# Kernel optimization log

Measured on AMD Instinct MI355X. Metric: run time of the kernel, lower is better.

The kernel has to match this reference:

```python
import jax, jax.numpy as jnp
import numpy as np

KERNEL_SIZE = 7  # must be odd
PAD = KERNEL_SIZE // 2


def setup_inputs() -> dict:
    key = jax.random.key(0)
    k1, k2 = jax.random.split(key)
    B, C, H, W = 8, 128, 256, 256
    x = jax.random.normal(k1, (B, C, H, W), dtype=jnp.float32)
    y = jax.random.normal(k2, (B, C, H, W), dtype=jnp.float32)
    return {"x": x, "y": y}


def reference(x, y):
    # x, y: [B, C, H, W] -> coef: [B, K*K, H, W]
    B, C, H, W = x.shape
    ypad = jnp.pad(y, ((0, 0), (0, 0), (PAD, PAD), (PAD, PAD)))  # ZeroPad2d
    coefs = []
    for i in range(KERNEL_SIZE):
        for j in range(KERNEL_SIZE):
            # shifted window of y, same spatial size as x
            yw = ypad[:, :, i:i + H, j:j + W]
            coefs.append(jnp.sum(x * yw, axis=1))  # channel dot product -> [B, H, W]
    return jnp.stack(coefs, axis=1)  # [B, K*K, H, W]
```

## Files before the change

kernel.cpp:

```cpp
#include <hip/hip_runtime.h>


#define Bq 8
#define Cq 128
#define Hq 256
#define Wq 256
#define Kq 7
#define TILE_H 8
#define TILE_W 64
#define NTHR 448

__global__ __launch_bounds__(NTHR)
void corr7_kernel(const float* __restrict__ x, const float* __restrict__ y,
                  float* __restrict__ out)
{
    const int t    = threadIdx.x;
    const int wave = t >> 6;
    const int lane = t & 63;
    const int lw   = lane & 7;
    const int lr   = lane >> 3;

    int bid = (int)blockIdx.x;
    bid = (bid & 7) * 128 + (bid >> 3);

    const int tw = bid & 3;
    const int th = (bid >> 2) & 31;
    const int b  = bid >> 7;

    const int h0 = th * TILE_H;
    const int w0 = tw * TILE_W;

    const size_t cs   = (size_t)Hq * Wq;
    const size_t base = (size_t)b * Cq * cs;

    const float* xp = x + base + (size_t)(h0 + lr) * Wq + (w0 + 8 * lw);

    const int gy    = h0 + lr + wave - 3;
    const bool rowok = (unsigned)gy < (unsigned)Hq;
    const float rowm = rowok ? 1.f : 0.f;
    const int gyc   = gy < 0 ? 0 : (gy > Hq - 1 ? Hq - 1 : gy);
    const float* yrow0 = y + base + (size_t)gyc * Wq;

    const int lanem1 = (lane + 63) & 63;
    const int lanep1 = (lane + 1) & 63;
    const bool isL = (lw == 0);
    const bool isR = (lw == 7);
    const float lm = (rowok && tw > 0) ? 1.f : 0.f;
    const float rm = (rowok && tw < 3) ? 1.f : 0.f;
    const int loff = (tw > 0) ? (w0 - 4) : w0;
    const int roff = (tw < 3) ? (w0 + TILE_W) : w0;

    float acc[Kq][8];
#pragma unroll
    for (int j = 0; j < Kq; ++j)
#pragma unroll
        for (int r = 0; r < 8; ++r) acc[j][r] = 0.f;

    for (int c = 0; c < Cq; ++c) {
        const size_t co = (size_t)c * cs;

        const float4 x0 = *(const float4*)(xp + co);
        const float4 x1 = *(const float4*)(xp + co + 4);

        const float* yr = yrow0 + co;
        float4 y0 = *(const float4*)(yr + w0 + 8 * lw);
        float4 y1 = *(const float4*)(yr + w0 + 8 * lw + 4);
        y0.x *= rowm; y0.y *= rowm; y0.z *= rowm; y0.w *= rowm;
        y1.x *= rowm; y1.y *= rowm; y1.z *= rowm; y1.w *= rowm;

        float4 hv = make_float4(0.f, 0.f, 0.f, 0.f);
        if (isL) hv = *(const float4*)(yr + loff);
        if (isR) hv = *(const float4*)(yr + roff);

        float l0 = __shfl(y1.y, lanem1);
        float l1 = __shfl(y1.z, lanem1);
        float l2 = __shfl(y1.w, lanem1);
        float r0 = __shfl(y0.x, lanep1);
        float r1 = __shfl(y0.y, lanep1);
        float r2 = __shfl(y0.z, lanep1);
        if (isL) { l0 = hv.y * lm; l1 = hv.z * lm; l2 = hv.w * lm; }
        if (isR) { r0 = hv.x * rm; r1 = hv.y * rm; r2 = hv.z * rm; }

        const float yw[14] = {l0, l1, l2,
                              y0.x, y0.y, y0.z, y0.w,
                              y1.x, y1.y, y1.z, y1.w,
                              r0, r1, r2};
        const float xv[8] = {x0.x, x0.y, x0.z, x0.w, x1.x, x1.y, x1.z, x1.w};
#pragma unroll
        for (int j = 0; j < Kq; ++j)
#pragma unroll
            for (int r = 0; r < 8; ++r)
                acc[j][r] = fmaf(xv[r], yw[r + j], acc[j][r]);
    }

    size_t obase = (((size_t)b * (Kq * Kq) + (size_t)wave * Kq) * Hq
                    + (h0 + lr)) * Wq + (w0 + 8 * lw);
#pragma unroll
    for (int j = 0; j < Kq; ++j) {
        float4 o0 = {acc[j][0], acc[j][1], acc[j][2], acc[j][3]};
        float4 o1 = {acc[j][4], acc[j][5], acc[j][6], acc[j][7]};
        *(float4*)(out + obase)     = o0;
        *(float4*)(out + obase + 4) = o1;
        obase += cs;
    }
}

extern "C" void kernel_launch(void* const* d_in, const int* in_sizes, int n_in,
                              void* d_out, int out_size, void* d_ws, size_t ws_size,
                              hipStream_t stream) {
    const float* x = (const float*)d_in[0];
    const float* y = (const float*)d_in[1];
    float* out = (float*)d_out;

    dim3 grid(Bq * 32 * 4);
    dim3 block(NTHR);
    hipLaunchKernelGGL(corr7_kernel, grid, block, 0, stream, x, y, out);
}
```

Measured before the change: 343.0 us.

## Recast channel correlation as bf16 MFMA matrix products over 16-wide pixel bands

Replaces the per-thread FP32 FMA correlation with MFMA 16x16x32 bf16 instructions. Each wave treats 16 output pixels against a 16+ wide band of shifted y pixels, reducing over channels in chunks of 32, and scatters only the 7 valid diagonals of each tile to the output. The grid is remapped to one image row per block across 4 column tiles. In exchange it converts inputs to bf16, which loses precision, computes many unused off-diagonal products, and loads scalar strided elements per channel instead of vector loads.

```diff
diff --git a/kernel.cpp b/kernel.cpp
--- a/kernel.cpp
+++ b/kernel.cpp
@@ -5,104 +5,129 @@
 #define Cq 128
 #define Hq 256
 #define Wq 256
-#define Kq 7
-#define TILE_H 8
-#define TILE_W 64
+#define CSq (Hq * Wq)
 #define NTHR 448
 
+typedef float f32x4 __attribute__((ext_vector_type(4)));
+typedef __bf16 bf16x8 __attribute__((ext_vector_type(8)));
+
+union Frag { unsigned u[4]; bf16x8 v; };
+
+__device__ __forceinline__ unsigned pkbf(float a, float b) {
+    union { __bf16 h[2]; unsigned u; } r;
+    r.h[0] = (__bf16)a; r.h[1] = (__bf16)b;
+    return r.u;
+}
+
+#define MFMA_(A, B, C) __builtin_amdgcn_mfma_f32_16x16x32_bf16((A), (B), (C), 0, 0, 0)
+
 __global__ __launch_bounds__(NTHR)
-void corr7_kernel(const float* __restrict__ x, const float* __restrict__ y,
-                  float* __restrict__ out)
+void corr7_mfma(const float* __restrict__ x, const float* __restrict__ y,
+                float* __restrict__ out)
 {
     const int t    = threadIdx.x;
     const int wave = t >> 6;
     const int lane = t & 63;
-    const int lw   = lane & 7;
-    const int lr   = lane >> 3;
+    const int g    = lane >> 4;
+    const int n    = lane & 15;
 
-    int bid = (int)blockIdx.x;
-    bid = (bid & 7) * 128 + (bid >> 3);
+    const int bid = (int)blockIdx.x;
+    const int b   = bid & 7;
+    const int id  = bid >> 3;
+    const int h   = id & 255;
+    const int w0  = (id >> 8) << 6;
 
-    const int tw = bid & 3;
-    const int th = (bid >> 2) & 31;
-    const int b  = bid >> 7;
+    const long base = (long)b * Cq * CSq;
 
-    const int h0 = th * TILE_H;
-    const int w0 = tw * TILE_W;
+    const int gy    = h + wave - 3;
+    const bool gyok = ((unsigned)gy < (unsigned)Hq);
+    const int gyc   = gyok ? gy : 0;
 
-    const size_t cs   = (size_t)Hq * Wq;
-    const size_t base = (size_t)b * Cq * cs;
+    const int d0 = (w0 == 0   && n < 4) ? (4 - n) : 0;
+    const int d4 = (w0 == 192 && n > 3) ? (3 - n) : 0;
 
-    const float* xp = x + base + (size_t)(h0 + lr) * Wq + (w0 + 8 * lw);
+    const unsigned mzM = gyok ? 0xFFFFFFFFu : 0u;
+    const unsigned mz0 = (gyok && d0 == 0) ? 0xFFFFFFFFu : 0u;
+    const unsigned mz4 = (gyok && d4 == 0) ? 0xFFFFFFFFu : 0u;
 
-    const int gy    = h0 + lr + wave - 3;
-    const bool rowok = (unsigned)gy < (unsigned)Hq;
-    const float rowm = rowok ? 1.f : 0.f;
-    const int gyc   = gy < 0 ? 0 : (gy > Hq - 1 ? Hq - 1 : gy);
-    const float* yrow0 = y + base + (size_t)gyc * Wq;
+#define CJ(J) (4 * g + ((J) & 3) + 16 * ((J) >> 2))
+    const long xrow = base + (long)h * Wq + (w0 + n);
+    const long yrow = base + (long)gyc * Wq + (w0 - 4 + n);
+    const float* px0 = x + xrow + (long)CJ(0) * CSq;
+    const float* px1 = x + xrow + (long)CJ(1) * CSq;
+    const float* px2 = x + xrow + (long)CJ(2) * CSq;
+    const float* px3 = x + xrow + (long)CJ(3) * CSq;
+    const float* px4 = x + xrow + (long)CJ(4) * CSq;
+    const float* px5 = x + xrow + (long)CJ(5) * CSq;
+    const float* px6 = x + xrow + (long)CJ(6) * CSq;
+    const float* px7 = x + xrow + (long)CJ(7) * CSq;
+    const float* py0 = y + yrow + (long)CJ(0) * CSq;
+    const float* py1 = y + yrow + (long)CJ(1) * CSq;
+    const float* py2 = y + yrow + (long)CJ(2) * CSq;
+    const float* py3 = y + yrow + (long)CJ(3) * CSq;
+    const float* py4 = y + yrow + (long)CJ(4) * CSq;
+    const float* py5 = y + yrow + (long)CJ(5) * CSq;
+    const float* py6 = y + yrow + (long)CJ(6) * CSq;
+    const float* py7 = y + yrow + (long)CJ(7) * CSq;
+#undef CJ
 
-    const int lanem1 = (lane + 63) & 63;
-    const int lanep1 = (lane + 1) & 63;
-    const bool isL = (lw == 0);
-    const bool isR = (lw == 7);
-    const float lm = (rowok && tw > 0) ? 1.f : 0.f;
-    const float rm = (rowok && tw < 3) ? 1.f : 0.f;
-    const int loff = (tw > 0) ? (w0 - 4) : w0;
-    const int roff = (tw < 3) ? (w0 + TILE_W) : w0;
+    f32x4 a00 = {0.f,0.f,0.f,0.f}, a01 = a00, a10 = a00, a11 = a00;
+    f32x4 a20 = a00, a21 = a00, a30 = a00, a31 = a00;
 
-    float acc[Kq][8];
-#pragma unroll
-    for (int j = 0; j < Kq; ++j)
-#pragma unroll
-        for (int r = 0; r < 8; ++r) acc[j][r] = 0.f;
+#define LOADX(F, OFF) { \
+    float t0 = px0[OFF], t1 = px1[OFF], t2 = px2[OFF], t3 = px3[OFF]; \
+    float t4 = px4[OFF], t5 = px5[OFF], t6 = px6[OFF], t7 = px7[OFF]; \
+    F.u[0] = pkbf(t0, t1); F.u[1] = pkbf(t2, t3); \
+    F.u[2] = pkbf(t4, t5); F.u[3] = pkbf(t6, t7); }
 
-    for (int c = 0; c < Cq; ++c) {
-        const size_t co = (size_t)c * cs;
+#define LOADY(F, OFF, MZ) { \
+    float t0 = py0[OFF], t1 = py1[OFF], t2 = py2[OFF], t3 = py3[OFF]; \
+    float t4 = py4[OFF], t5 = py5[OFF], t6 = py6[OFF], t7 = py7[OFF]; \
+    F.u[0] = pkbf(t0, t1) & (MZ); F.u[1] = pkbf(t2, t3) & (MZ); \
+    F.u[2] = pkbf(t4, t5) & (MZ); F.u[3] = pkbf(t6, t7) & (MZ); }
 
-        const float4 x0 = *(const float4*)(xp + co);
-        const float4 x1 = *(const float4*)(xp + co + 4);
+#pragma unroll 1
+    for (int kc = 0; kc < 4; ++kc) {
+        Frag A0, A1, A2, A3, B0, B1, B2, B3, B4;
+        LOADY(B0, d0, mz0)
+        LOADX(A0, 0)
+        LOADY(B1, 16, mzM)
+        LOADX(A1, 16)
+        a00 = MFMA_(A0.v, B0.v, a00);
+        a01 = MFMA_(A0.v, B1.v, a01);
+        LOADY(B2, 32, mzM)
+        LOADX(A2, 32)
+        a10 = MFMA_(A1.v, B1.v, a10);
+        a11 = MFMA_(A1.v, B2.v, a11);
+        LOADY(B3, 48, mzM)
+        LOADX(A3, 48)
+        a20 = MFMA_(A2.v, B2.v, a20);
+        a21 = MFMA_(A2.v, B3.v, a21);
+        LOADY(B4, 64 + d4, mz4)
+        a30 = MFMA_(A3.v, B3.v, a30);
+        a31 = MFMA_(A3.v, B4.v, a31);
+        px0 += 32L * CSq; px1 += 32L * CSq; px2 += 32L * CSq; px3 += 32L * CSq;
+        px4 += 32L * CSq; px5 += 32L * CSq; px6 += 32L * CSq; px7 += 32L * CSq;
+        py0 += 32L * CSq; py1 += 32L * CSq; py2 += 32L * CSq; py3 += 32L * CSq;
+        py4 += 32L * CSq; py5 += 32L * CSq; py6 += 32L * CSq; py7 += 32L * CSq;
+    }
+#undef LOADX
+#undef LOADY
 
-        const float* yr = yrow0 + co;
-        float4 y0 = *(const float4*)(yr + w0 + 8 * lw);
-        float4 y1 = *(const float4*)(yr + w0 + 8 * lw + 4);
-        y0.x *= rowm; y0.y *= rowm; y0.z *= rowm; y0.w *= rowm;
-        y1.x *= rowm; y1.y *= rowm; y1.z *= rowm; y1.w *= rowm;
-
-        float4 hv = make_float4(0.f, 0.f, 0.f, 0.f);
-        if (isL) hv = *(const float4*)(yr + loff);
-        if (isR) hv = *(const float4*)(yr + roff);
-
-        float l0 = __shfl(y1.y, lanem1);
-        float l1 = __shfl(y1.z, lanem1);
-        float l2 = __shfl(y1.w, lanem1);
-        float r0 = __shfl(y0.x, lanep1);
-        float r1 = __shfl(y0.y, lanep1);
-        float r2 = __shfl(y0.z, lanep1);
-        if (isL) { l0 = hv.y * lm; l1 = hv.z * lm; l2 = hv.w * lm; }
-        if (isR) { r0 = hv.x * rm; r1 = hv.y * rm; r2 = hv.z * rm; }
-
-        const float yw[14] = {l0, l1, l2,
-                              y0.x, y0.y, y0.z, y0.w,
-                              y1.x, y1.y, y1.z, y1.w,
-                              r0, r1, r2};
-        const float xv[8] = {x0.x, x0.y, x0.z, x0.w, x1.x, x1.y, x1.z, x1.w};
-#pragma unroll
-        for (int j = 0; j < Kq; ++j)
-#pragma unroll
-            for (int r = 0; r < 8; ++r)
-                acc[j][r] = fmaf(xv[r], yw[r + j], acc[j][r]);
-    }
-
-    size_t obase = (((size_t)b * (Kq * Kq) + (size_t)wave * Kq) * Hq
-                    + (h0 + lr)) * Wq + (w0 + 8 * lw);
-#pragma unroll
-    for (int j = 0; j < Kq; ++j) {
-        float4 o0 = {acc[j][0], acc[j][1], acc[j][2], acc[j][3]};
-        float4 o1 = {acc[j][4], acc[j][5], acc[j][6], acc[j][7]};
-        *(float4*)(out + obase)     = o0;
-        *(float4*)(out + obase + 4) = o1;
-        obase += cs;
-    }
+    const size_t ob = ((size_t)(b * 49 + 7 * wave)) * CSq
+                      + (size_t)h * Wq + w0;
+#define SCAT(ACC, MT, S) { \
+    _Pragma("unroll") \
+    for (int r = 0; r < 4; ++r) { \
+        const int dx = n + 16 * (S) - (4 * g + r) - 1; \
+        if ((unsigned)dx <= 6u) \
+            out[ob + (size_t)dx * CSq + 16 * (MT) + 4 * g + r] = (ACC)[r]; \
+    } }
+    SCAT(a00, 0, 0) SCAT(a01, 0, 1)
+    SCAT(a10, 1, 0) SCAT(a11, 1, 1)
+    SCAT(a20, 2, 0) SCAT(a21, 2, 1)
+    SCAT(a30, 3, 0) SCAT(a31, 3, 1)
+#undef SCAT
 }
 
 extern "C" void kernel_launch(void* const* d_in, const int* in_sizes, int n_in,
@@ -112,7 +137,7 @@
     const float* y = (const float*)d_in[1];
     float* out = (float*)d_out;
 
-    dim3 grid(Bq * 32 * 4);
+    dim3 grid(Bq * 256 * 4);
     dim3 block(NTHR);
-    hipLaunchKernelGGL(corr7_kernel, grid, block, 0, stream, x, y, out);
+    hipLaunchKernelGGL(corr7_mfma, grid, block, 0, stream, x, y, out);
 }
```

Measured after the change: 403.8 us. +17.7%, slower.
